# Performance work log

Hardware: AMD Instinct MI355X
Metric: run time of the kernel (lower is better)

Reference implementation:

```python
import jax, jax.numpy as jnp
import numpy as np

N = 50000    # nodes
E = 800000   # edges (avg degree 16)
DIN = 128    # input_dim
DH = 32      # hidden_dim (per-head channels)
H = 4        # heads


def setup_inputs() -> dict:
    key = jax.random.key(0)
    ks = jax.random.split(key, 32)
    inp = {}
    inp["x"] = jax.random.normal(ks[0], (N, DIN), dtype=jnp.float32)
    inp["edge_index"] = jax.random.randint(ks[1], (2, E), 0, N)
    # layer dims: (in, qkv_out, skip_out). Layers 0,1 concat heads (H*DH); layer 2 averages (DH).
    dims = [(DIN, H * DH, H * DH), (H * DH, H * DH, H * DH), (H * DH, H * DH, DH)]
    ki = 2
    for li, (din, dqkv, dskip) in enumerate(dims):
        for nm, do in (("q", dqkv), ("k", dqkv), ("v", dqkv), ("s", dskip)):
            inp[f"W{nm}{li}"] = jax.random.normal(ks[ki], (din, do), dtype=jnp.float32) * (1.0 / np.sqrt(din))
            ki += 1
            inp[f"b{nm}{li}"] = jax.random.normal(ks[ki], (do,), dtype=jnp.float32) * 0.01
            ki += 1
    return inp


def _transformer_conv(x, src, dst, Wq, bq, Wk, bk, Wv, bv, Ws, bs, concat):
    # PyG TransformerConv (beta=False, root_weight=True, eval mode -> no attn dropout)
    n = x.shape[0]
    q = (x @ Wq + bq).reshape(n, -1, DH)  # [N,H,d]
    k = (x @ Wk + bk).reshape(n, -1, DH)
    v = (x @ Wv + bv).reshape(n, -1, DH)
    # per-edge attention logits: q_i . k_j / sqrt(d), i=dst, j=src
    logits = jnp.einsum('ehd,ehd->eh', q[dst], k[src]) * (1.0 / np.sqrt(DH))  # [E,H]
    m = jax.ops.segment_max(logits, dst, num_segments=n)          # scatter-softmax max
    a = jnp.exp(logits - m[dst])
    s = jax.ops.segment_sum(a, dst, num_segments=n)
    alpha = a / s[dst]                                            # [E,H]
    msg = v[src] * alpha[..., None]                               # [E,H,d]
    agg = jax.ops.segment_sum(msg.reshape(msg.shape[0], -1), dst, num_segments=n)
    agg = agg.reshape(n, -1, DH)
    out = agg.reshape(n, -1) if concat else agg.mean(axis=1)
    return out + x @ Ws + bs  # root/skip connection


def reference(x, edge_index,
              Wq0, bq0, Wk0, bk0, Wv0, bv0, Ws0, bs0,
              Wq1, bq1, Wk1, bk1, Wv1, bv1, Ws1, bs1,
              Wq2, bq2, Wk2, bk2, Wv2, bv2, Ws2, bs2):
    src, dst = edge_index[0], edge_index[1]
    h = _transformer_conv(x, src, dst, Wq0, bq0, Wk0, bk0, Wv0, bv0, Ws0, bs0, True)
    h = jax.nn.relu(h)  # dropout is identity in eval
    h = _transformer_conv(h, src, dst, Wq1, bq1, Wk1, bk1, Wv1, bv1, Ws1, bs1, True)
    h = jax.nn.relu(h)
    out = _transformer_conv(h, src, dst, Wq2, bq2, Wk2, bk2, Wv2, bv2, Ws2, bs2, False)
    return out  # [N, DH]
```

## Files before the change

kernel.cpp:

```cpp
#include <hip/hip_runtime.h>
#include <cstdint>
#include <cstddef>

#define DIN 128
#define ROW_BYTES 1024

typedef __attribute__((ext_vector_type(8))) short short8v;
typedef __attribute__((ext_vector_type(4))) float float4v;

__global__ void k_count(const int* __restrict__ dst, int* __restrict__ deg, int E){
  int i = blockIdx.x*blockDim.x + threadIdx.x;
  if(i<E) atomicAdd(&deg[dst[i]], 1);
}

__global__ void k_scan1(const int* __restrict__ deg, int* __restrict__ offs,
                        int* __restrict__ part, int n){
  __shared__ int sm[256];
  int t = threadIdx.x; int g = blockIdx.x*256 + t;
  int v = (g<n)? deg[g] : 0;
  sm[t] = v;
  for(int o=1;o<256;o<<=1){
    __syncthreads();
    int x = (t>=o)? sm[t-o] : 0;
    __syncthreads();
    sm[t] += x;
  }
  __syncthreads();
  if(g<n) offs[g+1] = sm[t];
  if(t==255) part[blockIdx.x] = sm[255];
}

__global__ void k_scan2(int* __restrict__ part, int nb){
  __shared__ int sm[256];
  int t=threadIdx.x;
  int v = (t<nb)? part[t] : 0;
  sm[t]=v;
  for(int o=1;o<256;o<<=1){ __syncthreads(); int x=(t>=o)?sm[t-o]:0; __syncthreads(); sm[t]+=x; }
  __syncthreads();
  if(t<nb) part[t] = sm[t]-v;
}

__global__ void k_scan3(int* __restrict__ offs, const int* __restrict__ part, int n){
  int t=threadIdx.x; int g=blockIdx.x*256+t;
  if(g<n) offs[g+1] += part[blockIdx.x];
  if(g==0) offs[0]=0;
}

__global__ void k_scatter(const int* __restrict__ src, const int* __restrict__ dst,
                          const int* __restrict__ offs, int* __restrict__ cur,
                          int* __restrict__ srcs, int E){
  int i=blockIdx.x*blockDim.x+threadIdx.x;
  if(i<E){
    int d = dst[i];
    int p = atomicAdd(&cur[d],1);
    srcs[offs[d]+p] = src[i];
  }
}

__device__ inline unsigned f2bf(float x){
  unsigned u = __float_as_uint(x);
  return (u + 0x7FFFu + ((u>>16)&1u)) >> 16;
}
__device__ inline unsigned pack2(float a, float b){ return f2bf(a) | (f2bf(b)<<16); }
__device__ inline float bflo(unsigned w){ return __uint_as_float(w<<16); }
__device__ inline float bfhi(unsigned w){ return __uint_as_float(w & 0xFFFF0000u); }

__global__ void k_wt(
  const float* __restrict__ W0, const float* __restrict__ W1, const float* __restrict__ W2,
  const float* __restrict__ W3, const float* __restrict__ W4, const float* __restrict__ W5,
  const float* __restrict__ W6, const float* __restrict__ W7, const float* __restrict__ W8,
  const float* __restrict__ W9, const float* __restrict__ W10, const float* __restrict__ W11,
  unsigned short* __restrict__ wt)
{
  int i = blockIdx.y;
  int e = blockIdx.x*256 + threadIdx.x;
  int dout = (i==11)? 32 : 128;
  if(e >= dout*128) return;
  const float* W;
  switch(i){
    case 0: W=W0; break; case 1: W=W1; break; case 2: W=W2; break; case 3: W=W3; break;
    case 4: W=W4; break; case 5: W=W5; break; case 6: W=W6; break; case 7: W=W7; break;
    case 8: W=W8; break; case 9: W=W9; break; case 10: W=W10; break; default: W=W11; break;
  }
  int c = e % dout, k = e / dout;
  wt[i*16384 + c*128 + k] = (unsigned short)f2bf(W[(size_t)k*dout + c]);
}

__global__ __launch_bounds__(256,4) void k_gemm(
  const void* __restrict__ Xv, int xbf, int nrows,
  const unsigned short* __restrict__ Wt,
  const float* __restrict__ bq, const float* __restrict__ bk,
  const float* __restrict__ bv, const float* __restrict__ bs,
  int ws_cols, char* __restrict__ out)
{
  __shared__ unsigned short Xs[64][136];
  __shared__ unsigned short Wsh[64][136];
  int t = threadIdx.x;
  int row0 = blockIdx.x*64;
  {
    int r = t>>2, kb = (t&3)*32;
    int gr = row0 + r;
    if(gr < nrows){
      if(xbf){
        const unsigned short* xp = (const unsigned short*)Xv + (size_t)gr*DIN + kb;
        #pragma unroll
        for(int j=0;j<4;j++)
          *(uint4*)&Xs[r][kb + j*8] = *(const uint4*)(xp + j*8);
      } else {
        const float* xp = (const float*)Xv + (size_t)gr*DIN + kb;
        #pragma unroll
        for(int j=0;j<4;j++){
          float4 fa = *(const float4*)(xp + j*8);
          float4 fb = *(const float4*)(xp + j*8 + 4);
          uint4 pk = make_uint4(pack2(fa.x,fa.y), pack2(fa.z,fa.w),
                                pack2(fb.x,fb.y), pack2(fb.z,fb.w));
          *(uint4*)&Xs[r][kb + j*8] = pk;
        }
      }
    } else {
      uint4 z = make_uint4(0,0,0,0);
      #pragma unroll
      for(int j=0;j<4;j++) *(uint4*)&Xs[r][kb + j*8] = z;
    }
  }
  int wv = t>>6, l = t&63;
  int lr = l & 15, lk = (l>>4)*8;
  for(int mat=0; mat<4; mat++){
    int wcols = (mat==3)? ws_cols : 128;
    const unsigned short* Wm = Wt + mat*16384;
    const float* bias = (mat==0)?bq:(mat==1)?bk:(mat==2)?bv:bs;
    for(int half=0; half<2; half++){
      int col0 = half*64;
      if(col0 >= wcols) break;
      {
        int c = t>>2, kb = (t&3)*32;
        int gc = col0 + c;
        if(gc < wcols){
          const unsigned short* wp = Wm + (size_t)gc*128 + kb;
          #pragma unroll
          for(int j=0;j<4;j++)
            *(uint4*)&Wsh[c][kb + j*8] = *(const uint4*)(wp + j*8);
        } else {
          uint4 z = make_uint4(0,0,0,0);
          #pragma unroll
          for(int j=0;j<4;j++) *(uint4*)&Wsh[c][kb + j*8] = z;
        }
      }
      __syncthreads();
      float4v acc[4];
      #pragma unroll
      for(int mt=0;mt<4;mt++) acc[mt] = (float4v){0.f,0.f,0.f,0.f};
      #pragma unroll
      for(int kk=0;kk<4;kk++){
        short8v b = *(const short8v*)&Wsh[wv*16 + lr][kk*32 + lk];
        #pragma unroll
        for(int mt=0;mt<4;mt++){
          short8v a = *(const short8v*)&Xs[mt*16 + lr][kk*32 + lk];
          acc[mt] = __builtin_amdgcn_mfma_f32_16x16x32_bf16(a, b, acc[mt], 0, 0, 0);
        }
      }
      int col = col0 + wv*16 + lr;
      bool cok = col < wcols;
      float bcol = cok ? bias[col] : 0.f;
      int rb = row0 + (l>>4)*4;
      #pragma unroll
      for(int mt=0;mt<4;mt++){
        #pragma unroll
        for(int j=0;j<4;j++){
          int r = rb + mt*16 + j;
          if(r < nrows && cok){
            float val = acc[mt][j] + bcol;
            char* rowp = out + ((size_t)r<<10);
            if(mat==0)      *(unsigned short*)(rowp + col*2) = (unsigned short)f2bf(val);
            else if(mat==3) *(unsigned short*)(rowp + 768 + col*2) = (unsigned short)f2bf(val);
            else {
              int h = col>>5, d = col&31;
              int off = ((mat==1)?256:512) + (d>>3)*64 + h*16 + (d&7)*2;
              *(unsigned short*)(rowp + off) = (unsigned short)f2bf(val);
            }
          }
        }
      }
      __syncthreads();
    }
  }
}

__global__ __launch_bounds__(256,4) void k_attn(
  const char* __restrict__ QKVS, const int* __restrict__ offs,
  const int* __restrict__ srcs, void* __restrict__ outv, int mode, int n)
{
  int wv = threadIdx.x>>6, lane = threadIdx.x&63;
  int node = blockIdx.x*4 + wv;
  if(node >= n) return;
  int h = lane & 3;
  int e_l = lane >> 2;
  const float rs = 0.17677669529663687f;
  const char* rowq = QKVS + ((size_t)node<<10) + h*64;
  uint4 qw[4];
  #pragma unroll
  for(int j=0;j<4;j++) qw[j] = *(const uint4*)(rowq + j*16);
  int beg = offs[node], end = offs[node+1];
  float m = 0.f, s = 0.f;
  float4 acc[8];
  #pragma unroll
  for(int j=0;j<8;j++) acc[j] = make_float4(0.f,0.f,0.f,0.f);

  if(beg < end){
    {
      int idx = beg + e_l;
      bool msk = idx < end;
      int sj = srcs[msk ? idx : beg];
      const char* base = QKVS + ((size_t)sj<<10) + 256 + h*16;
      uint4 vw[4];
      #pragma unroll
      for(int j=0;j<4;j++) vw[j] = *(const uint4*)(base + 256 + j*64);
      #pragma unroll
      for(int j=0;j<4;j++)
        asm volatile("" : "+v"(vw[j].x), "+v"(vw[j].y), "+v"(vw[j].z), "+v"(vw[j].w));
      float dot = 0.f;
      #pragma unroll
      for(int j=0;j<4;j++){
        uint4 kwj = *(const uint4*)(base + j*64);
        uint4 qj = qw[j];
        dot += bflo(qj.x)*bflo(kwj.x) + bfhi(qj.x)*bfhi(kwj.x)
             + bflo(qj.y)*bflo(kwj.y) + bfhi(qj.y)*bfhi(kwj.y)
             + bflo(qj.z)*bflo(kwj.z) + bfhi(qj.z)*bfhi(kwj.z)
             + bflo(qj.w)*bflo(kwj.w) + bfhi(qj.w)*bfhi(kwj.w);
      }
      dot *= rs;
      float logit = msk ? dot : -__builtin_inff();
      float bm = logit;
      bm = fmaxf(bm, __shfl_xor(bm,4));
      bm = fmaxf(bm, __shfl_xor(bm,8));
      bm = fmaxf(bm, __shfl_xor(bm,16));
      bm = fmaxf(bm, __shfl_xor(bm,32));
      float p = __expf(logit - bm);
      float ps = p;
      ps += __shfl_xor(ps,4); ps += __shfl_xor(ps,8); ps += __shfl_xor(ps,16); ps += __shfl_xor(ps,32);
      s = ps; m = bm;
      #pragma unroll
      for(int j=0;j<4;j++){
        uint4 w = vw[j];
        acc[2*j]   = make_float4(p*bflo(w.x), p*bfhi(w.x), p*bflo(w.y), p*bfhi(w.y));
        acc[2*j+1] = make_float4(p*bflo(w.z), p*bfhi(w.z), p*bflo(w.w), p*bfhi(w.w));
      }
    }
    for(int b0 = beg+16; b0 < end; b0 += 16){
      int idx = b0 + e_l;
      bool msk = idx < end;
      int sj = srcs[msk ? idx : beg];
      const char* base = QKVS + ((size_t)sj<<10) + 256 + h*16;
      uint4 vw[4];
      #pragma unroll
      for(int j=0;j<4;j++) vw[j] = *(const uint4*)(base + 256 + j*64);
      #pragma unroll
      for(int j=0;j<4;j++)
        asm volatile("" : "+v"(vw[j].x), "+v"(vw[j].y), "+v"(vw[j].z), "+v"(vw[j].w));
      float dot = 0.f;
      #pragma unroll
      for(int j=0;j<4;j++){
        uint4 kwj = *(const uint4*)(base + j*64);
        uint4 qj = qw[j];
        dot += bflo(qj.x)*bflo(kwj.x) + bfhi(qj.x)*bfhi(kwj.x)
             + bflo(qj.y)*bflo(kwj.y) + bfhi(qj.y)*bfhi(kwj.y)
             + bflo(qj.z)*bflo(kwj.z) + bfhi(qj.z)*bfhi(kwj.z)
             + bflo(qj.w)*bflo(kwj.w) + bfhi(qj.w)*bfhi(kwj.w);
      }
      dot *= rs;
      float logit = msk ? dot : -__builtin_inff();
      float bm = logit;
      bm = fmaxf(bm, __shfl_xor(bm,4));
      bm = fmaxf(bm, __shfl_xor(bm,8));
      bm = fmaxf(bm, __shfl_xor(bm,16));
      bm = fmaxf(bm, __shfl_xor(bm,32));
      float mn = fmaxf(m, bm);
      float r = __expf(m - mn);
      float p = __expf(logit - mn);
      float ps = p;
      ps += __shfl_xor(ps,4); ps += __shfl_xor(ps,8); ps += __shfl_xor(ps,16); ps += __shfl_xor(ps,32);
      s = r*s + ps; m = mn;
      #pragma unroll
      for(int j=0;j<4;j++){
        uint4 w = vw[j];
        float4 a0 = acc[2*j], a1 = acc[2*j+1];
        a0.x = fmaf(a0.x, r, p*bflo(w.x)); a0.y = fmaf(a0.y, r, p*bfhi(w.x));
        a0.z = fmaf(a0.z, r, p*bflo(w.y)); a0.w = fmaf(a0.w, r, p*bfhi(w.y));
        a1.x = fmaf(a1.x, r, p*bflo(w.z)); a1.y = fmaf(a1.y, r, p*bfhi(w.z));
        a1.z = fmaf(a1.z, r, p*bflo(w.w)); a1.w = fmaf(a1.w, r, p*bfhi(w.w));
        acc[2*j] = a0; acc[2*j+1] = a1;
      }
    }
  }
  int b5 = (lane>>5)&1, b4 = (lane>>4)&1, b3 = (lane>>3)&1, b2 = (lane>>2)&1;
  float4 r4[4];
  #pragma unroll
  for(int j=0;j<4;j++){
    float4 keep = b5 ? acc[j+4] : acc[j];
    float4 send = b5 ? acc[j]   : acc[j+4];
    keep.x += __shfl_xor(send.x,32); keep.y += __shfl_xor(send.y,32);
    keep.z += __shfl_xor(send.z,32); keep.w += __shfl_xor(send.w,32);
    r4[j] = keep;
  }
  float4 r2[2];
  #pragma unroll
  for(int j=0;j<2;j++){
    float4 keep = b4 ? r4[j+2] : r4[j];
    float4 send = b4 ? r4[j]   : r4[j+2];
    keep.x += __shfl_xor(send.x,16); keep.y += __shfl_xor(send.y,16);
    keep.z += __shfl_xor(send.z,16); keep.w += __shfl_xor(send.w,16);
    r2[j] = keep;
  }
  float4 r1;
  {
    float4 keep = b3 ? r2[1] : r2[0];
    float4 send = b3 ? r2[0] : r2[1];
    keep.x += __shfl_xor(send.x,8); keep.y += __shfl_xor(send.y,8);
    keep.z += __shfl_xor(send.z,8); keep.w += __shfl_xor(send.w,8);
    r1 = keep;
  }
  float fx, fy;
  {
    float kx = b2 ? r1.z : r1.x, ky = b2 ? r1.w : r1.y;
    float sx = b2 ? r1.x : r1.z, sy = b2 ? r1.y : r1.w;
    fx = kx + __shfl_xor(sx,4);
    fy = ky + __shfl_xor(sy,4);
  }
  float inv = (s > 0.f) ? (1.f/s) : 0.f;
  if(mode == 0){
    unsigned sw = *(const unsigned*)(QKVS + ((size_t)node<<10) + 768 + h*64 + e_l*4);
    float ox = fmaxf(fmaf(fx, inv, bflo(sw)), 0.f);
    float oy = fmaxf(fmaf(fy, inv, bfhi(sw)), 0.f);
    ((unsigned*)outv)[(size_t)node*64 + h*16 + e_l] = pack2(ox, oy);
  } else {
    float sc = inv*0.25f;
    float ox = fx*sc, oy = fy*sc;
    ox += __shfl_xor(ox,1); oy += __shfl_xor(oy,1);
    ox += __shfl_xor(ox,2); oy += __shfl_xor(oy,2);
    if(h == 0){
      unsigned sw = *(const unsigned*)(QKVS + ((size_t)node<<10) + 768 + e_l*4);
      float* op = (float*)outv + (size_t)node*32 + 2*e_l;
      op[0] = ox + bflo(sw); op[1] = oy + bfhi(sw);
    }
  }
}

extern "C" void kernel_launch(void* const* d_in, const int* in_sizes, int n_in,
                              void* d_out, int out_size, void* d_ws, size_t ws_size,
                              hipStream_t stream) {
  const float* x = (const float*)d_in[0];
  const int* ei = (const int*)d_in[1];
  int n = in_sizes[0]/DIN;
  int E = in_sizes[1]/2;
  const int* esrc = ei;
  const int* edst = ei + E;

  char* w = (char*)d_ws;
  auto alloc = [&](size_t bytes)->char*{
    char* p = w; w += (bytes + 255) & ~(size_t)255; return p;
  };
  int* offs = (int*)alloc((size_t)(n+1)*4);
  int* deg  = (int*)alloc((size_t)n*4);
  int* cur  = (int*)alloc((size_t)n*4);
  int* part = (int*)alloc(256*4);
  int* srcs = (int*)alloc((size_t)E*4);
  char* qkvs = alloc((size_t)n*ROW_BYTES);
  unsigned short* h1 = (unsigned short*)alloc((size_t)n*128*2);
  unsigned short* h2 = (unsigned short*)alloc((size_t)n*128*2);
  unsigned short* wt = (unsigned short*)alloc((size_t)12*16384*2);

  auto f = [&](int i)->const float*{ return (const float*)d_in[i]; };

  hipLaunchKernelGGL(k_wt, dim3(64,12), dim3(256), 0, stream,
                     f(2),f(4),f(6),f(8), f(10),f(12),f(14),f(16), f(18),f(20),f(22),f(24), wt);

  int SB = (n+255)/256;
  hipMemsetAsync(deg, 0, (size_t)n*4, stream);
  hipMemsetAsync(cur, 0, (size_t)n*4, stream);
  hipLaunchKernelGGL(k_count, dim3((E+255)/256), dim3(256), 0, stream, edst, deg, E);
  hipLaunchKernelGGL(k_scan1, dim3(SB), dim3(256), 0, stream, deg, offs, part, n);
  hipLaunchKernelGGL(k_scan2, dim3(1), dim3(256), 0, stream, part, SB);
  hipLaunchKernelGGL(k_scan3, dim3(SB), dim3(256), 0, stream, offs, part, n);
  hipLaunchKernelGGL(k_scatter, dim3((E+255)/256), dim3(256), 0, stream, esrc, edst, offs, cur, srcs, E);

  int RT = (n+63)/64;
  int AB = (n+3)/4;

  hipLaunchKernelGGL(k_gemm, dim3(RT), dim3(256), 0, stream,
                     (const void*)x, 0, n, wt + 0*4*16384, f(3),f(5),f(7),f(9), 128, qkvs);
  hipLaunchKernelGGL(k_attn, dim3(AB), dim3(256), 0, stream, qkvs, offs, srcs, (void*)h1, 0, n);
  hipLaunchKernelGGL(k_gemm, dim3(RT), dim3(256), 0, stream,
                     (const void*)h1, 1, n, wt + 1*4*16384, f(11),f(13),f(15),f(17), 128, qkvs);
  hipLaunchKernelGGL(k_attn, dim3(AB), dim3(256), 0, stream, qkvs, offs, srcs, (void*)h2, 0, n);
  hipLaunchKernelGGL(k_gemm, dim3(RT), dim3(256), 0, stream,
                     (const void*)h2, 1, n, wt + 2*4*16384, f(19),f(21),f(23),f(25), 32, qkvs);
  hipLaunchKernelGGL(k_attn, dim3(AB), dim3(256), 0, stream, qkvs, offs, srcs, d_out, 1, n);
}
```

Baseline: 419.1 us.

## Prefetch GEMM weight tiles in registers and simplify attention softmax without max

New measurement: 453.1 us. +8.1%, slower.

```diff
diff --git a/kernel.cpp b/kernel.cpp
--- a/kernel.cpp
+++ b/kernel.cpp
@@ -97,15 +97,15 @@
   __shared__ unsigned short Wsh[64][136];
   int t = threadIdx.x;
   int row0 = blockIdx.x*64;
+  int c = t>>2, kb = (t&3)*32;
   {
-    int r = t>>2, kb = (t&3)*32;
-    int gr = row0 + r;
+    int gr = row0 + c;
     if(gr < nrows){
       if(xbf){
         const unsigned short* xp = (const unsigned short*)Xv + (size_t)gr*DIN + kb;
         #pragma unroll
         for(int j=0;j<4;j++)
-          *(uint4*)&Xs[r][kb + j*8] = *(const uint4*)(xp + j*8);
+          *(uint4*)&Xs[c][kb + j*8] = *(const uint4*)(xp + j*8);
       } else {
         const float* xp = (const float*)Xv + (size_t)gr*DIN + kb;
         #pragma unroll
@@ -114,84 +114,88 @@
           float4 fb = *(const float4*)(xp + j*8 + 4);
           uint4 pk = make_uint4(pack2(fa.x,fa.y), pack2(fa.z,fa.w),
                                 pack2(fb.x,fb.y), pack2(fb.z,fb.w));
-          *(uint4*)&Xs[r][kb + j*8] = pk;
+          *(uint4*)&Xs[c][kb + j*8] = pk;
         }
       }
     } else {
       uint4 z = make_uint4(0,0,0,0);
       #pragma unroll
-      for(int j=0;j<4;j++) *(uint4*)&Xs[r][kb + j*8] = z;
+      for(int j=0;j<4;j++) *(uint4*)&Xs[c][kb + j*8] = z;
     }
   }
   int wv = t>>6, l = t&63;
   int lr = l & 15, lk = (l>>4)*8;
-  for(int mat=0; mat<4; mat++){
+  int P = (ws_cols > 64) ? 8 : 7;
+  uint4 w0, w1, w2, w3;
+  {
+    const unsigned short* wp = Wt + (size_t)c*128 + kb;
+    w0 = *(const uint4*)(wp);
+    w1 = *(const uint4*)(wp + 8);
+    w2 = *(const uint4*)(wp + 16);
+    w3 = *(const uint4*)(wp + 24);
+  }
+  for(int p=0; p<P; p++){
+    int mat = p>>1, half = p&1;
     int wcols = (mat==3)? ws_cols : 128;
-    const unsigned short* Wm = Wt + mat*16384;
-    const float* bias = (mat==0)?bq:(mat==1)?bk:(mat==2)?bv:bs;
-    for(int half=0; half<2; half++){
-      int col0 = half*64;
-      if(col0 >= wcols) break;
-      {
-        int c = t>>2, kb = (t&3)*32;
-        int gc = col0 + c;
-        if(gc < wcols){
-          const unsigned short* wp = Wm + (size_t)gc*128 + kb;
-          #pragma unroll
-          for(int j=0;j<4;j++)
-            *(uint4*)&Wsh[c][kb + j*8] = *(const uint4*)(wp + j*8);
-        } else {
-          uint4 z = make_uint4(0,0,0,0);
-          #pragma unroll
-          for(int j=0;j<4;j++) *(uint4*)&Wsh[c][kb + j*8] = z;
-        }
-      }
-      __syncthreads();
-      float4v acc[4];
-      #pragma unroll
-      for(int mt=0;mt<4;mt++) acc[mt] = (float4v){0.f,0.f,0.f,0.f};
-      #pragma unroll
-      for(int kk=0;kk<4;kk++){
-        short8v b = *(const short8v*)&Wsh[wv*16 + lr][kk*32 + lk];
-        #pragma unroll
-        for(int mt=0;mt<4;mt++){
-          short8v a = *(const short8v*)&Xs[mt*16 + lr][kk*32 + lk];
-          acc[mt] = __builtin_amdgcn_mfma_f32_16x16x32_bf16(a, b, acc[mt], 0, 0, 0);
-        }
-      }
-      int col = col0 + wv*16 + lr;
-      bool cok = col < wcols;
-      float bcol = cok ? bias[col] : 0.f;
-      int rb = row0 + (l>>4)*4;
+    int col0 = half*64;
+    __syncthreads();
+    *(uint4*)&Wsh[c][kb]      = w0;
+    *(uint4*)&Wsh[c][kb + 8]  = w1;
+    *(uint4*)&Wsh[c][kb + 16] = w2;
+    *(uint4*)&Wsh[c][kb + 24] = w3;
+    if(p+1 < P){
+      int m2 = (p+1)>>1, h2 = (p+1)&1;
+      const unsigned short* wp = Wt + m2*16384 + (size_t)(h2*64 + c)*128 + kb;
+      w0 = *(const uint4*)(wp);
+      w1 = *(const uint4*)(wp + 8);
+      w2 = *(const uint4*)(wp + 16);
+      w3 = *(const uint4*)(wp + 24);
+    }
+    __syncthreads();
+    float4v acc[4];
+    #pragma unroll
+    for(int mt=0;mt<4;mt++) acc[mt] = (float4v){0.f,0.f,0.f,0.f};
+    #pragma unroll
+    for(int kk=0;kk<4;kk++){
+      short8v b = *(const short8v*)&Wsh[wv*16 + lr][kk*32 + lk];
       #pragma unroll
       for(int mt=0;mt<4;mt++){
-        #pragma unroll
-        for(int j=0;j<4;j++){
-          int r = rb + mt*16 + j;
-          if(r < nrows && cok){
-            float val = acc[mt][j] + bcol;
-            char* rowp = out + ((size_t)r<<10);
-            if(mat==0)      *(unsigned short*)(rowp + col*2) = (unsigned short)f2bf(val);
-            else if(mat==3) *(unsigned short*)(rowp + 768 + col*2) = (unsigned short)f2bf(val);
-            else {
-              int h = col>>5, d = col&31;
-              int off = ((mat==1)?256:512) + (d>>3)*64 + h*16 + (d&7)*2;
-              *(unsigned short*)(rowp + off) = (unsigned short)f2bf(val);
-            }
+        short8v a = *(const short8v*)&Xs[mt*16 + lr][kk*32 + lk];
+        acc[mt] = __builtin_amdgcn_mfma_f32_16x16x32_bf16(a, b, acc[mt], 0, 0, 0);
+      }
+    }
+    const float* bias = (mat==0)?bq:(mat==1)?bk:(mat==2)?bv:bs;
+    int col = col0 + wv*16 + lr;
+    bool cok = col < wcols;
+    float bcol = cok ? bias[col] : 0.f;
+    int rb = row0 + (l>>4)*4;
+    #pragma unroll
+    for(int mt=0;mt<4;mt++){
+      #pragma unroll
+      for(int j=0;j<4;j++){
+        int r = rb + mt*16 + j;
+        if(r < nrows && cok){
+          float val = acc[mt][j] + bcol;
+          char* rowp = out + ((size_t)r<<10);
+          if(mat==0)      *(unsigned short*)(rowp + col*2) = (unsigned short)f2bf(val);
+          else if(mat==3) *(unsigned short*)(rowp + 768 + col*2) = (unsigned short)f2bf(val);
+          else {
+            int h = col>>5, d = col&31;
+            int off = ((mat==1)?256:512) + (d>>3)*64 + h*16 + (d&7)*2;
+            *(unsigned short*)(rowp + off) = (unsigned short)f2bf(val);
           }
         }
       }
-      __syncthreads();
-    }
-  }
-}
-
-__global__ __launch_bounds__(256,4) void k_attn(
+    }
+  }
+}
+
+__global__ __launch_bounds__(64,4) void k_attn(
   const char* __restrict__ QKVS, const int* __restrict__ offs,
   const int* __restrict__ srcs, void* __restrict__ outv, int mode, int n)
 {
-  int wv = threadIdx.x>>6, lane = threadIdx.x&63;
-  int node = blockIdx.x*4 + wv;
+  int lane = threadIdx.x;
+  int node = blockIdx.x;
   if(node >= n) return;
   int h = lane & 3;
   int e_l = lane >> 2;
@@ -201,95 +205,45 @@
   #pragma unroll
   for(int j=0;j<4;j++) qw[j] = *(const uint4*)(rowq + j*16);
   int beg = offs[node], end = offs[node+1];
-  float m = 0.f, s = 0.f;
+  float s = 0.f;
   float4 acc[8];
   #pragma unroll
   for(int j=0;j<8;j++) acc[j] = make_float4(0.f,0.f,0.f,0.f);
 
-  if(beg < end){
-    {
-      int idx = beg + e_l;
-      bool msk = idx < end;
-      int sj = srcs[msk ? idx : beg];
-      const char* base = QKVS + ((size_t)sj<<10) + 256 + h*16;
-      uint4 vw[4];
-      #pragma unroll
-      for(int j=0;j<4;j++) vw[j] = *(const uint4*)(base + 256 + j*64);
-      #pragma unroll
-      for(int j=0;j<4;j++)
-        asm volatile("" : "+v"(vw[j].x), "+v"(vw[j].y), "+v"(vw[j].z), "+v"(vw[j].w));
-      float dot = 0.f;
-      #pragma unroll
-      for(int j=0;j<4;j++){
-        uint4 kwj = *(const uint4*)(base + j*64);
-        uint4 qj = qw[j];
-        dot += bflo(qj.x)*bflo(kwj.x) + bfhi(qj.x)*bfhi(kwj.x)
-             + bflo(qj.y)*bflo(kwj.y) + bfhi(qj.y)*bfhi(kwj.y)
-             + bflo(qj.z)*bflo(kwj.z) + bfhi(qj.z)*bfhi(kwj.z)
-             + bflo(qj.w)*bflo(kwj.w) + bfhi(qj.w)*bfhi(kwj.w);
-      }
-      dot *= rs;
-      float logit = msk ? dot : -__builtin_inff();
-      float bm = logit;
-      bm = fmaxf(bm, __shfl_xor(bm,4));
-      bm = fmaxf(bm, __shfl_xor(bm,8));
-      bm = fmaxf(bm, __shfl_xor(bm,16));
-      bm = fmaxf(bm, __shfl_xor(bm,32));
-      float p = __expf(logit - bm);
-      float ps = p;
-      ps += __shfl_xor(ps,4); ps += __shfl_xor(ps,8); ps += __shfl_xor(ps,16); ps += __shfl_xor(ps,32);
-      s = ps; m = bm;
-      #pragma unroll
-      for(int j=0;j<4;j++){
-        uint4 w = vw[j];
-        acc[2*j]   = make_float4(p*bflo(w.x), p*bfhi(w.x), p*bflo(w.y), p*bfhi(w.y));
-        acc[2*j+1] = make_float4(p*bflo(w.z), p*bfhi(w.z), p*bflo(w.w), p*bfhi(w.w));
-      }
-    }
-    for(int b0 = beg+16; b0 < end; b0 += 16){
-      int idx = b0 + e_l;
-      bool msk = idx < end;
-      int sj = srcs[msk ? idx : beg];
-      const char* base = QKVS + ((size_t)sj<<10) + 256 + h*16;
-      uint4 vw[4];
-      #pragma unroll
-      for(int j=0;j<4;j++) vw[j] = *(const uint4*)(base + 256 + j*64);
-      #pragma unroll
-      for(int j=0;j<4;j++)
-        asm volatile("" : "+v"(vw[j].x), "+v"(vw[j].y), "+v"(vw[j].z), "+v"(vw[j].w));
-      float dot = 0.f;
-      #pragma unroll
-      for(int j=0;j<4;j++){
-        uint4 kwj = *(const uint4*)(base + j*64);
-        uint4 qj = qw[j];
-        dot += bflo(qj.x)*bflo(kwj.x) + bfhi(qj.x)*bfhi(kwj.x)
-             + bflo(qj.y)*bflo(kwj.y) + bfhi(qj.y)*bfhi(kwj.y)
-             + bflo(qj.z)*bflo(kwj.z) + bfhi(qj.z)*bfhi(kwj.z)
-             + bflo(qj.w)*bflo(kwj.w) + bfhi(qj.w)*bfhi(kwj.w);
-      }
-      dot *= rs;
-      float logit = msk ? dot : -__builtin_inff();
-      float bm = logit;
-      bm = fmaxf(bm, __shfl_xor(bm,4));
-      bm = fmaxf(bm, __shfl_xor(bm,8));
-      bm = fmaxf(bm, __shfl_xor(bm,16));
-      bm = fmaxf(bm, __shfl_xor(bm,32));
-      float mn = fmaxf(m, bm);
-      float r = __expf(m - mn);
-      float p = __expf(logit - mn);
-      float ps = p;
-      ps += __shfl_xor(ps,4); ps += __shfl_xor(ps,8); ps += __shfl_xor(ps,16); ps += __shfl_xor(ps,32);
-      s = r*s + ps; m = mn;
-      #pragma unroll
-      for(int j=0;j<4;j++){
-        uint4 w = vw[j];
-        float4 a0 = acc[2*j], a1 = acc[2*j+1];
-        a0.x = fmaf(a0.x, r, p*bflo(w.x)); a0.y = fmaf(a0.y, r, p*bfhi(w.x));
-        a0.z = fmaf(a0.z, r, p*bflo(w.y)); a0.w = fmaf(a0.w, r, p*bfhi(w.y));
-        a1.x = fmaf(a1.x, r, p*bflo(w.z)); a1.y = fmaf(a1.y, r, p*bfhi(w.z));
-        a1.z = fmaf(a1.z, r, p*bflo(w.w)); a1.w = fmaf(a1.w, r, p*bfhi(w.w));
-        acc[2*j] = a0; acc[2*j+1] = a1;
-      }
+  for(int b0 = beg; b0 < end; b0 += 16){
+    int idx = b0 + e_l;
+    bool msk = idx < end;
+    int sj = srcs[msk ? idx : beg];
+    const char* base = QKVS + ((size_t)sj<<10) + 256 + h*16;
+    uint4 vw[4];
+    #pragma unroll
+    for(int j=0;j<4;j++) vw[j] = *(const uint4*)(base + 256 + j*64);
+    #pragma unroll
+    for(int j=0;j<4;j++)
+      asm volatile("" : "+v"(vw[j].x), "+v"(vw[j].y), "+v"(vw[j].z), "+v"(vw[j].w));
+    float dot = 0.f;
+    #pragma unroll
+    for(int j=0;j<4;j++){
+      uint4 kwj = *(const uint4*)(base + j*64);
+      uint4 qj = qw[j];
+      dot += bflo(qj.x)*bflo(kwj.x) + bfhi(qj.x)*bfhi(kwj.x)
+           + bflo(qj.y)*bflo(kwj.y) + bfhi(qj.y)*bfhi(kwj.y)
+           + bflo(qj.z)*bflo(kwj.z) + bfhi(qj.z)*bfhi(kwj.z)
+           + bflo(qj.w)*bflo(kwj.w) + bfhi(qj.w)*bfhi(kwj.w);
+    }
+    float p = msk ? __expf(dot * rs) : 0.f;
+    float ps = p;
+    ps += __shfl_xor(ps,4); ps += __shfl_xor(ps,8); ps += __shfl_xor(ps,16); ps += __shfl_xor(ps,32);
+    s += ps;
+    #pragma unroll
+    for(int j=0;j<4;j++){
+      uint4 w = vw[j];
+      float4 a0 = acc[2*j], a1 = acc[2*j+1];
+      a0.x = fmaf(p, bflo(w.x), a0.x); a0.y = fmaf(p, bfhi(w.x), a0.y);
+      a0.z = fmaf(p, bflo(w.y), a0.z); a0.w = fmaf(p, bfhi(w.y), a0.w);
+      a1.x = fmaf(p, bflo(w.z), a1.x); a1.y = fmaf(p, bfhi(w.z), a1.y);
+      a1.z = fmaf(p, bflo(w.w), a1.z); a1.w = fmaf(p, bfhi(w.w), a1.w);
+      acc[2*j] = a0; acc[2*j+1] = a1;
     }
   }
   int b5 = (lane>>5)&1, b4 = (lane>>4)&1, b3 = (lane>>3)&1, b2 = (lane>>2)&1;
@@ -384,15 +338,14 @@
   hipLaunchKernelGGL(k_scatter, dim3((E+255)/256), dim3(256), 0, stream, esrc, edst, offs, cur, srcs, E);
 
   int RT = (n+63)/64;
-  int AB = (n+3)/4;
 
   hipLaunchKernelGGL(k_gemm, dim3(RT), dim3(256), 0, stream,
                      (const void*)x, 0, n, wt + 0*4*16384, f(3),f(5),f(7),f(9), 128, qkvs);
-  hipLaunchKernelGGL(k_attn, dim3(AB), dim3(256), 0, stream, qkvs, offs, srcs, (void*)h1, 0, n);
+  hipLaunchKernelGGL(k_attn, dim3(n), dim3(64), 0, stream, qkvs, offs, srcs, (void*)h1, 0, n);
   hipLaunchKernelGGL(k_gemm, dim3(RT), dim3(256), 0, stream,
                      (const void*)h1, 1, n, wt + 1*4*16384, f(11),f(13),f(15),f(17), 128, qkvs);
-  hipLaunchKernelGGL(k_attn, dim3(AB), dim3(256), 0, stream, qkvs, offs, srcs, (void*)h2, 0, n);
+  hipLaunchKernelGGL(k_attn, dim3(n), dim3(64), 0, stream, qkvs, offs, srcs, (void*)h2, 0, n);
   hipLaunchKernelGGL(k_gemm, dim3(RT), dim3(256), 0, stream,
                      (const void*)h2, 1, n, wt + 2*4*16384, f(19),f(21),f(23),f(25), 32, qkvs);
-  hipLaunchKernelGGL(k_attn, dim3(AB), dim3(256), 0, stream, qkvs, offs, srcs, d_out, 1, n);
-}
+  hipLaunchKernelGGL(k_attn, dim3(n), dim3(64), 0, stream, qkvs, offs, srcs, d_out, 1, n);
+}
```

## Software-pipeline weight tile loads in GEMM and prefetch next edge rows in attention

Applied to the files above, without the earlier changes.

Result: no change. 417.1 us (-0.5%).

```diff
diff --git a/kernel.cpp b/kernel.cpp
--- a/kernel.cpp
+++ b/kernel.cpp
@@ -97,15 +97,15 @@
   __shared__ unsigned short Wsh[64][136];
   int t = threadIdx.x;
   int row0 = blockIdx.x*64;
+  int c = t>>2, kb = (t&3)*32;
   {
-    int r = t>>2, kb = (t&3)*32;
-    int gr = row0 + r;
+    int gr = row0 + c;
     if(gr < nrows){
       if(xbf){
         const unsigned short* xp = (const unsigned short*)Xv + (size_t)gr*DIN + kb;
         #pragma unroll
         for(int j=0;j<4;j++)
-          *(uint4*)&Xs[r][kb + j*8] = *(const uint4*)(xp + j*8);
+          *(uint4*)&Xs[c][kb + j*8] = *(const uint4*)(xp + j*8);
       } else {
         const float* xp = (const float*)Xv + (size_t)gr*DIN + kb;
         #pragma unroll
@@ -114,74 +114,78 @@
           float4 fb = *(const float4*)(xp + j*8 + 4);
           uint4 pk = make_uint4(pack2(fa.x,fa.y), pack2(fa.z,fa.w),
                                 pack2(fb.x,fb.y), pack2(fb.z,fb.w));
-          *(uint4*)&Xs[r][kb + j*8] = pk;
+          *(uint4*)&Xs[c][kb + j*8] = pk;
         }
       }
     } else {
       uint4 z = make_uint4(0,0,0,0);
       #pragma unroll
-      for(int j=0;j<4;j++) *(uint4*)&Xs[r][kb + j*8] = z;
+      for(int j=0;j<4;j++) *(uint4*)&Xs[c][kb + j*8] = z;
     }
   }
   int wv = t>>6, l = t&63;
   int lr = l & 15, lk = (l>>4)*8;
-  for(int mat=0; mat<4; mat++){
+  int P = (ws_cols > 64) ? 8 : 7;
+  uint4 w0, w1, w2, w3;
+  {
+    const unsigned short* wp = Wt + (size_t)c*128 + kb;
+    w0 = *(const uint4*)(wp);
+    w1 = *(const uint4*)(wp + 8);
+    w2 = *(const uint4*)(wp + 16);
+    w3 = *(const uint4*)(wp + 24);
+  }
+  for(int p=0; p<P; p++){
+    int mat = p>>1, half = p&1;
     int wcols = (mat==3)? ws_cols : 128;
-    const unsigned short* Wm = Wt + mat*16384;
+    int col0 = half*64;
+    __syncthreads();
+    *(uint4*)&Wsh[c][kb]      = w0;
+    *(uint4*)&Wsh[c][kb + 8]  = w1;
+    *(uint4*)&Wsh[c][kb + 16] = w2;
+    *(uint4*)&Wsh[c][kb + 24] = w3;
+    if(p+1 < P){
+      int m2 = (p+1)>>1, h2 = (p+1)&1;
+      const unsigned short* wp = Wt + m2*16384 + (size_t)(h2*64 + c)*128 + kb;
+      w0 = *(const uint4*)(wp);
+      w1 = *(const uint4*)(wp + 8);
+      w2 = *(const uint4*)(wp + 16);
+      w3 = *(const uint4*)(wp + 24);
+    }
+    __syncthreads();
+    float4v acc[4];
+    #pragma unroll
+    for(int mt=0;mt<4;mt++) acc[mt] = (float4v){0.f,0.f,0.f,0.f};
+    #pragma unroll
+    for(int kk=0;kk<4;kk++){
+      short8v b = *(const short8v*)&Wsh[wv*16 + lr][kk*32 + lk];
+      #pragma unroll
+      for(int mt=0;mt<4;mt++){
+        short8v a = *(const short8v*)&Xs[mt*16 + lr][kk*32 + lk];
+        acc[mt] = __builtin_amdgcn_mfma_f32_16x16x32_bf16(a, b, acc[mt], 0, 0, 0);
+      }
+    }
     const float* bias = (mat==0)?bq:(mat==1)?bk:(mat==2)?bv:bs;
-    for(int half=0; half<2; half++){
-      int col0 = half*64;
-      if(col0 >= wcols) break;
-      {
-        int c = t>>2, kb = (t&3)*32;
-        int gc = col0 + c;
-        if(gc < wcols){
-          const unsigned short* wp = Wm + (size_t)gc*128 + kb;
-          #pragma unroll
-          for(int j=0;j<4;j++)
-            *(uint4*)&Wsh[c][kb + j*8] = *(const uint4*)(wp + j*8);
-        } else {
-          uint4 z = make_uint4(0,0,0,0);
-          #pragma unroll
-          for(int j=0;j<4;j++) *(uint4*)&Wsh[c][kb + j*8] = z;
-        }
-      }
-      __syncthreads();
-      float4v acc[4];
-      #pragma unroll
-      for(int mt=0;mt<4;mt++) acc[mt] = (float4v){0.f,0.f,0.f,0.f};
-      #pragma unroll
-      for(int kk=0;kk<4;kk++){
-        short8v b = *(const short8v*)&Wsh[wv*16 + lr][kk*32 + lk];
-        #pragma unroll
-        for(int mt=0;mt<4;mt++){
-          short8v a = *(const short8v*)&Xs[mt*16 + lr][kk*32 + lk];
-          acc[mt] = __builtin_amdgcn_mfma_f32_16x16x32_bf16(a, b, acc[mt], 0, 0, 0);
-        }
-      }
-      int col = col0 + wv*16 + lr;
-      bool cok = col < wcols;
-      float bcol = cok ? bias[col] : 0.f;
-      int rb = row0 + (l>>4)*4;
-      #pragma unroll
-      for(int mt=0;mt<4;mt++){
-        #pragma unroll
-        for(int j=0;j<4;j++){
-          int r = rb + mt*16 + j;
-          if(r < nrows && cok){
-            float val = acc[mt][j] + bcol;
-            char* rowp = out + ((size_t)r<<10);
-            if(mat==0)      *(unsigned short*)(rowp + col*2) = (unsigned short)f2bf(val);
-            else if(mat==3) *(unsigned short*)(rowp + 768 + col*2) = (unsigned short)f2bf(val);
-            else {
-              int h = col>>5, d = col&31;
-              int off = ((mat==1)?256:512) + (d>>3)*64 + h*16 + (d&7)*2;
-              *(unsigned short*)(rowp + off) = (unsigned short)f2bf(val);
-            }
+    int col = col0 + wv*16 + lr;
+    bool cok = col < wcols;
+    float bcol = cok ? bias[col] : 0.f;
+    int rb = row0 + (l>>4)*4;
+    #pragma unroll
+    for(int mt=0;mt<4;mt++){
+      #pragma unroll
+      for(int j=0;j<4;j++){
+        int r = rb + mt*16 + j;
+        if(r < nrows && cok){
+          float val = acc[mt][j] + bcol;
+          char* rowp = out + ((size_t)r<<10);
+          if(mat==0)      *(unsigned short*)(rowp + col*2) = (unsigned short)f2bf(val);
+          else if(mat==3) *(unsigned short*)(rowp + 768 + col*2) = (unsigned short)f2bf(val);
+          else {
+            int h = col>>5, d = col&31;
+            int off = ((mat==1)?256:512) + (d>>3)*64 + h*16 + (d&7)*2;
+            *(unsigned short*)(rowp + off) = (unsigned short)f2bf(val);
           }
         }
       }
-      __syncthreads();
     }
   }
 }
@@ -228,6 +232,14 @@
              + bflo(qj.z)*bflo(kwj.z) + bfhi(qj.z)*bfhi(kwj.z)
              + bflo(qj.w)*bflo(kwj.w) + bfhi(qj.w)*bfhi(kwj.w);
       }
+      if(beg + 16 < end){
+        int i2 = beg + 16 + e_l;
+        int sj2 = srcs[(i2 < end) ? i2 : beg];
+        const char* rp = QKVS + ((size_t)sj2<<10);
+        unsigned pfk = *(const unsigned*)(rp + 256 + h*64);
+        unsigned pfv = *(const unsigned*)(rp + 512 + h*64);
+        asm volatile("" : "+v"(pfk), "+v"(pfv));
+      }
       dot *= rs;
       float logit = msk ? dot : -__builtin_inff();
       float bm = logit;
@@ -266,6 +278,14 @@
              + bflo(qj.y)*bflo(kwj.y) + bfhi(qj.y)*bfhi(kwj.y)
              + bflo(qj.z)*bflo(kwj.z) + bfhi(qj.z)*bfhi(kwj.z)
              + bflo(qj.w)*bflo(kwj.w) + bfhi(qj.w)*bfhi(kwj.w);
+      }
+      if(b0 + 16 < end){
+        int i2 = b0 + 16 + e_l;
+        int sj2 = srcs[(i2 < end) ? i2 : beg];
+        const char* rp = QKVS + ((size_t)sj2<<10);
+        unsigned pfk = *(const unsigned*)(rp + 256 + h*64);
+        unsigned pfv = *(const unsigned*)(rp + 512 + h*64);
+        asm volatile("" : "+v"(pfk), "+v"(pfv));
       }
       dot *= rs;
       float logit = msk ? dot : -__builtin_inff();
```
